# Kernel optimization log

Measured on AMD Instinct MI355X. Metric: run time of the kernel, lower is better.

Reference implementation:

```python
import jax, jax.numpy as jnp
import numpy as np

EPS = 1e-12  # matches torch F.normalize default eps


def _idx(k, pad, stride, size):
    o = (size + 2 * pad - k) // stride + 1
    return (jnp.arange(o) * stride)[:, None] + jnp.arange(k)[None, :], o  # [o, k]


def unfold(x, k, pad, stride):
    # x: [B, C, H, W] -> [B, C*k*k, oh*ow], torch F.unfold ordering (c slowest, then kh, kw)
    B, C, H, W = x.shape
    xp = jnp.pad(x, ((0, 0), (0, 0), (pad, pad), (pad, pad)))
    ri, oh = _idx(k, pad, stride, H)
    ci, ow = _idx(k, pad, stride, W)
    p = xp[:, :, ri[:, None, :, None], ci[None, :, None, :]]  # [B, C, oh, ow, k, k]
    return p.transpose(0, 1, 4, 5, 2, 3).reshape(B, C * k * k, oh * ow)


def fold(cols, out_hw, k, pad, stride):
    # inverse of unfold with overlap-add (torch F.fold)
    B, CKK, L = cols.shape
    C = CKK // (k * k)
    H, W = out_hw
    ri, oh = _idx(k, pad, stride, H)
    ci, ow = _idx(k, pad, stride, W)
    p = cols.reshape(B, C, k, k, oh, ow).transpose(0, 1, 4, 5, 2, 3)  # [B,C,oh,ow,k,k]
    canvas = jnp.zeros((B, C, H + 2 * pad, W + 2 * pad), cols.dtype)
    canvas = canvas.at[:, :, ri[:, None, :, None], ci[None, :, None, :]].add(p)
    return canvas[:, :, pad:pad + H, pad:pad + W]


def _l2norm(x, axis):
    n = jnp.sqrt(jnp.sum(x * x, axis=axis, keepdims=True))
    return x / jnp.maximum(n, EPS)


def setup_inputs() -> dict:
    key = jax.random.key(0)
    ks = jax.random.split(key, 5)
    return {
        "lrsr_lv3": jax.random.normal(ks[0], (1, 256, 48, 48), jnp.float32),
        "refsr_lv3": jax.random.normal(ks[1], (1, 256, 48, 48), jnp.float32),
        "ref_lv1": jax.random.normal(ks[2], (1, 64, 192, 192), jnp.float32),
        "ref_lv2": jax.random.normal(ks[3], (1, 128, 96, 96), jnp.float32),
        "ref_lv3": jax.random.normal(ks[4], (1, 256, 48, 48), jnp.float32),
    }


def reference(lrsr_lv3, refsr_lv3, ref_lv1, ref_lv2, ref_lv3):
    B, C, H, W = lrsr_lv3.shape
    lr_u = unfold(lrsr_lv3, 3, 1, 1)              # [B, C*9, L_lr]
    rf_u = unfold(refsr_lv3, 3, 1, 1)             # [B, C*9, L_ref]
    rf_n = _l2norm(rf_u.transpose(0, 2, 1), 2)    # [B, L_ref, C*9]
    lr_n = _l2norm(lr_u, 1)                       # [B, C*9, L_lr]
    R = jnp.einsum('brc,bcl->brl', rf_n, lr_n)    # [B, L_ref, L_lr] cosine corr
    R_star = jnp.max(R, axis=1)                   # [B, L_lr]
    R_arg = jnp.argmax(R, axis=1)                 # [B, L_lr]

    ref3_u = unfold(ref_lv3, 3, 1, 1)             # [B, C*9,   L_ref]
    ref2_u = unfold(ref_lv2, 6, 2, 2)             # [B, C2*36, L_ref]
    ref1_u = unfold(ref_lv1, 12, 4, 4)            # [B, C1*144,L_ref]

    idx = R_arg[:, None, :]                       # [B, 1, L_lr]
    T3_u = jnp.take_along_axis(ref3_u, idx, axis=2)
    T2_u = jnp.take_along_axis(ref2_u, idx, axis=2)
    T1_u = jnp.take_along_axis(ref1_u, idx, axis=2)

    T_lv3 = fold(T3_u, (H, W), 3, 1, 1) / 9.0
    T_lv2 = fold(T2_u, (H * 2, W * 2), 6, 2, 2) / 9.0
    T_lv1 = fold(T1_u, (H * 4, W * 4), 12, 4, 4) / 9.0
    S = R_star.reshape(B, 1, H, W)
    return (S, T_lv3, T_lv2, T_lv1)
```

## Files before the change

### kernel.cpp

```cpp
#include <hip/hip_runtime.h>
#include <hip/hip_bf16.h>
#include <math.h>

#define HW 48
#define NPOS 2304
#define CCH 256
#define PCOLS 2500
#define PLANESZ (NPOS * CCH)
#define KC 16
#define TM 128
#define TN 64

typedef __attribute__((ext_vector_type(8))) short short8v;
typedef __attribute__((ext_vector_type(16))) float f32x16;

__device__ inline void ph_ss2(int vb, const float* __restrict__ lr,
                              const float* __restrict__ ref, float* __restrict__ SS2,
                              float (*red)[64]) {
    const int img = vb / 36, bx = vb % 36;
    const float* imgp = img ? ref : lr;
    const int t = threadIdx.x;
    const int px = t & 63, cg = t >> 6;
    const int p = bx * 64 + px;
    const float* base = imgp + (size_t)cg * 64 * NPOS + p;
    float s = 0.f;
#pragma unroll 4
    for (int cc = 0; cc < 64; ++cc) {
        float v = base[(size_t)cc * NPOS];
        s = fmaf(v, v, s);
    }
    red[cg][px] = s;
    __syncthreads();
    if (cg == 0)
        SS2[img * NPOS + p] = red[0][px] + red[1][px] + red[2][px] + red[3][px];
}

__device__ inline void ph_split(int local, const float* __restrict__ lr,
                                const float* __restrict__ ref, ushort* __restrict__ planes) {
    const int img = local / 288;
    const int gid = (local % 288) * 256 + threadIdx.x;
    const float* src = img ? ref : lr;
    const int lane = gid & 63;
    const int k16  = (gid >> 6) & 15;
    const int blk  = gid >> 10;
    const int pos  = blk * 32 + (lane & 31);
    const int c0   = k16 * 16 + (lane >> 5) * 8;
    ushort h8[8], m8[8], l8[8];
#pragma unroll
    for (int e = 0; e < 8; ++e) {
        float a = src[(size_t)(c0 + e) * NPOS + pos];
        __hip_bfloat16 hb = __float2bfloat16(a);
        float hf = __bfloat162float(hb);
        float r1 = a - hf;
        __hip_bfloat16 mb = __float2bfloat16(r1);
        float mf = __bfloat162float(mb);
        __hip_bfloat16 lb = __float2bfloat16(r1 - mf);
        h8[e] = *(ushort*)&hb;
        m8[e] = *(ushort*)&mb;
        l8[e] = *(ushort*)&lb;
    }
    ushort* ph = planes + (size_t)(img * 3 + 0) * PLANESZ + (size_t)gid * 8;
    ushort* pm = planes + (size_t)(img * 3 + 1) * PLANESZ + (size_t)gid * 8;
    ushort* pl = planes + (size_t)(img * 3 + 2) * PLANESZ + (size_t)gid * 8;
#pragma unroll
    for (int e = 0; e < 8; ++e) { ph[e] = h8[e]; pm[e] = m8[e]; pl[e] = l8[e]; }
}

__device__ inline void ph_zero(int local, float* __restrict__ P) {
    const int idx = local * 256 + threadIdx.x;
    if (idx >= NPOS * 196) return;
    const int row = idx / 196, b = idx - row * 196;
    int pc;
    if (b < 50)       pc = b;
    else if (b < 100) pc = 2450 + (b - 50);
    else {
        const int i = b - 100;
        const int rr = 1 + (i >> 1);
        pc = rr * 50 + ((i & 1) ? 49 : 0);
    }
    P[(size_t)row * PCOLS + pc] = 0.f;
}

__global__ __launch_bounds__(256) void prep_kernel(const float* __restrict__ lr,
                                                   const float* __restrict__ ref,
                                                   float* __restrict__ SS2,
                                                   ushort* __restrict__ planes,
                                                   float* __restrict__ P,
                                                   int do_split) {
    __shared__ float red[4][64];
    const int b = blockIdx.x;
    if (do_split) {
        if (b < 72)        ph_ss2(b, lr, ref, SS2, red);
        else if (b < 648)  ph_split(b - 72, lr, ref, planes);
        else               ph_zero(b - 648, P);
    } else {
        if (b < 72)        ph_ss2(b, lr, ref, SS2, red);
        else               ph_zero(b - 72, P);
    }
}

__device__ inline void ph_invnorm(int vb, const float* __restrict__ SS2,
                                  float* __restrict__ inv2) {
    const int img = vb / 9;
    const int p = (vb % 9) * 256 + threadIdx.x;
    const float* SS = SS2 + img * NPOS;
    const int y = p / HW, x = p % HW;
    float s = 0.f;
#pragma unroll
    for (int di = -1; di <= 1; ++di) {
        int yy = y + di;
        if ((unsigned)yy >= HW) continue;
#pragma unroll
        for (int dj = -1; dj <= 1; ++dj) {
            int xx = x + dj;
            if ((unsigned)xx >= HW) continue;
            s += SS[yy * HW + xx];
        }
    }
    inv2[img * NPOS + p] = 1.f / fmaxf(sqrtf(s), 1e-12f);
}

__device__ inline void ph_gemm(int g, const ushort* __restrict__ planes,
                               float* __restrict__ P) {
    const int bxg = g % 36, byg = g / 36;
    const int t = threadIdx.x, lane = t & 63, w = t >> 6;
    const int nblk0 = bxg * 2;
    const int ablk  = byg * 4 + w;

    const ushort* baseA  = planes + ((size_t)(ablk * 16) * 64 + lane) * 8;
    const ushort* baseB0 = planes + (size_t)3 * PLANESZ + ((size_t)(nblk0 * 16) * 64 + lane) * 8;
    const ushort* baseB1 = baseB0 + 16 * 64 * 8;

    f32x16 acc0 = {};
    f32x16 acc1 = {};
#pragma unroll 4
    for (int k = 0; k < 16; ++k) {
        const int fo = k * 512;
        short8v ah = *(const short8v*)(baseA + fo);
        short8v am = *(const short8v*)(baseA + PLANESZ + fo);
        short8v al = *(const short8v*)(baseA + 2 * PLANESZ + fo);
        short8v bh0 = *(const short8v*)(baseB0 + fo);
        short8v bm0 = *(const short8v*)(baseB0 + PLANESZ + fo);
        short8v bl0 = *(const short8v*)(baseB0 + 2 * PLANESZ + fo);
        short8v bh1 = *(const short8v*)(baseB1 + fo);
        short8v bm1 = *(const short8v*)(baseB1 + PLANESZ + fo);
        short8v bl1 = *(const short8v*)(baseB1 + 2 * PLANESZ + fo);
        acc0 = __builtin_amdgcn_mfma_f32_32x32x16_bf16(ah, bh0, acc0, 0, 0, 0);
        acc0 = __builtin_amdgcn_mfma_f32_32x32x16_bf16(ah, bm0, acc0, 0, 0, 0);
        acc0 = __builtin_amdgcn_mfma_f32_32x32x16_bf16(am, bh0, acc0, 0, 0, 0);
        acc0 = __builtin_amdgcn_mfma_f32_32x32x16_bf16(ah, bl0, acc0, 0, 0, 0);
        acc0 = __builtin_amdgcn_mfma_f32_32x32x16_bf16(al, bh0, acc0, 0, 0, 0);
        acc0 = __builtin_amdgcn_mfma_f32_32x32x16_bf16(am, bm0, acc0, 0, 0, 0);
        acc1 = __builtin_amdgcn_mfma_f32_32x32x16_bf16(ah, bh1, acc1, 0, 0, 0);
        acc1 = __builtin_amdgcn_mfma_f32_32x32x16_bf16(ah, bm1, acc1, 0, 0, 0);
        acc1 = __builtin_amdgcn_mfma_f32_32x32x16_bf16(am, bh1, acc1, 0, 0, 0);
        acc1 = __builtin_amdgcn_mfma_f32_32x32x16_bf16(ah, bl1, acc1, 0, 0, 0);
        acc1 = __builtin_amdgcn_mfma_f32_32x32x16_bf16(al, bh1, acc1, 0, 0, 0);
        acc1 = __builtin_amdgcn_mfma_f32_32x32x16_bf16(am, bm1, acc1, 0, 0, 0);
    }
    const int m0 = byg * 128 + w * 32;
    const int half = lane >> 5;
    const int colA = nblk0 * 32 + (lane & 31);
    const int colB = colA + 32;
    const int pcA = (colA / 48) * 50 + colA % 48 + 51;
    const int pcB = (colB / 48) * 50 + colB % 48 + 51;
#pragma unroll
    for (int r = 0; r < 16; ++r) {
        const int row = (r & 3) + 8 * (r >> 2) + 4 * half;
        P[(size_t)(m0 + row) * PCOLS + pcA] = acc0[r];
        P[(size_t)(m0 + row) * PCOLS + pcB] = acc1[r];
    }
}

__global__ __launch_bounds__(256) void corr_kernel(const float* __restrict__ SS2,
                                                   float* __restrict__ inv2,
                                                   const ushort* __restrict__ planes,
                                                   float* __restrict__ P,
                                                   int do_gemm) {
    const int b = blockIdx.x;
    if (b < 18)          ph_invnorm(b, SS2, inv2);
    else if (do_gemm)    ph_gemm(b - 18, planes, P);
}

__global__ __launch_bounds__(256) void gemm_p_kernel(const float* __restrict__ lr,
                                                     const float* __restrict__ ref,
                                                     float* __restrict__ P) {
    __shared__ float As[KC][TM];
    __shared__ float Bs[KC][TN];
    const int t  = threadIdx.x;
    const int tx = t & 15, ty = t >> 4;
    const int lp0 = blockIdx.y * TM, rp0 = blockIdx.x * TN;
    const int ac0 = t >> 5,        acol0 = (t & 31) << 2;
    const int ac1 = (t + 256) >> 5, acol1 = acol0;
    const int bc = t >> 4, bcol = (t & 15) << 2;
    float acc[8][4] = {};
    for (int c0 = 0; c0 < CCH; c0 += KC) {
        float4 a0 = *(const float4*)(lr  + (size_t)(c0 + ac0) * NPOS + lp0 + acol0);
        float4 a1 = *(const float4*)(lr  + (size_t)(c0 + ac1) * NPOS + lp0 + acol1);
        float4 b0 = *(const float4*)(ref + (size_t)(c0 + bc)  * NPOS + rp0 + bcol);
        __syncthreads();
        *(float4*)&As[ac0][acol0] = a0;
        *(float4*)&As[ac1][acol1] = a1;
        *(float4*)&Bs[bc][bcol]   = b0;
        __syncthreads();
#pragma unroll
        for (int kk = 0; kk < KC; ++kk) {
            float4 aA = *(const float4*)&As[kk][ty * 8];
            float4 aB = *(const float4*)&As[kk][ty * 8 + 4];
            float4 bb = *(const float4*)&Bs[kk][tx * 4];
            const float av[8] = {aA.x, aA.y, aA.z, aA.w, aB.x, aB.y, aB.z, aB.w};
            const float bv[4] = {bb.x, bb.y, bb.z, bb.w};
#pragma unroll
            for (int i = 0; i < 8; ++i)
#pragma unroll
                for (int j = 0; j < 4; ++j)
                    acc[i][j] = fmaf(av[i], bv[j], acc[i][j]);
        }
    }
    const int col0 = rp0 + tx * 4;
    const int pc0  = (col0 / 48) * 50 + (col0 % 48) + 51;
#pragma unroll
    for (int i = 0; i < 8; ++i) {
        const int m = lp0 + ty * 8 + i;
        float4 v = make_float4(acc[i][0], acc[i][1], acc[i][2], acc[i][3]);
        __builtin_memcpy(P + (size_t)m * PCOLS + pc0, &v, 16);
    }
}

__global__ __launch_bounds__(192) void maxarg_kernel(const float* __restrict__ P,
                                                     const float* __restrict__ inr,
                                                     const float* __restrict__ inl,
                                                     float* __restrict__ S,
                                                     int* __restrict__ arg) {
    const int l  = blockIdx.x;
    const int yl = l / HW, xl = l % HW;
    const int t  = threadIdx.x;

    bool vmask[9];
    const float* bp[9];
#pragma unroll
    for (int d = 0; d < 9; ++d) {
        const int di = d / 3 - 1, dj = d % 3 - 1;
        vmask[d] = ((unsigned)(yl + di) < HW) && ((unsigned)(xl + dj) < HW);
        bp[d] = P + (ptrdiff_t)(l + di * HW + dj) * PCOLS + (di * 50 + dj);
    }

    float best = -1e30f;
    int bestr = 0;
#pragma unroll
    for (int vv = 0; vv < 3; ++vv) {
        const int v   = t + vv * 192;
        const int yr  = v / 12;
        const int xr4 = (v - yr * 12) << 2;
        const int q0  = yr * 50 + xr4 + 51;
        const int r0  = yr * HW + xr4;
        float4 a = make_float4(0.f, 0.f, 0.f, 0.f);
#pragma unroll
        for (int d = 0; d < 9; ++d) {
            if (vmask[d]) {
                float4 x;
                __builtin_memcpy(&x, bp[d] + q0, 16);
                a.x += x.x; a.y += x.y; a.z += x.z; a.w += x.w;
            }
        }
        const float4 w = *(const float4*)(inr + r0);
        const float vals[4] = {a.x * w.x, a.y * w.y, a.z * w.z, a.w * w.w};
#pragma unroll
        for (int k = 0; k < 4; ++k)
            if (vals[k] > best) { best = vals[k]; bestr = r0 + k; }
    }

    __shared__ float bv[256];
    __shared__ int   br[256];
    bv[t] = best; br[t] = bestr;
    if (t < 64) { bv[192 + t] = -1e30f; br[192 + t] = 0; }
    __syncthreads();
    for (int s2 = 128; s2 > 0; s2 >>= 1) {
        if (t < s2) {
            float v2 = bv[t + s2]; int r2 = br[t + s2];
            if (v2 > bv[t] || (v2 == bv[t] && r2 < br[t])) { bv[t] = v2; br[t] = r2; }
        }
        __syncthreads();
    }
    if (t == 0) {
        S[l]   = bv[0] * inl[l];
        arg[l] = br[0];
    }
}

__global__ __launch_bounds__(256) void transposeT_kernel(const float* __restrict__ ref1,
                                                         const float* __restrict__ ref2,
                                                         const float* __restrict__ ref3,
                                                         float* __restrict__ T3t,
                                                         float* __restrict__ T2t,
                                                         float* __restrict__ T1t) {
    __shared__ float tile[64][65];
    const int b = blockIdx.x;
    const float* src; float* dst; int C, NPIX, tpx, tch;
    if (b < 144)      { src = ref3; dst = T3t; C = 256; NPIX = 2304;  tpx = b % 36;  tch = b / 36; }
    else if (b < 432) { const int lb = b - 144; src = ref2; dst = T2t; C = 128; NPIX = 9216;  tpx = lb % 144; tch = lb / 144; }
    else              { const int lb = b - 432; src = ref1; dst = T1t; C = 64;  NPIX = 36864; tpx = lb;       tch = 0; }
    const int t = threadIdx.x;
    const int px0 = tpx * 64, c0 = tch * 64;
#pragma unroll
    for (int r = 0; r < 16; ++r) {
        const int cl = r * 4 + (t >> 6), pl = t & 63;
        tile[cl][pl] = src[(size_t)(c0 + cl) * NPIX + px0 + pl];
    }
    __syncthreads();
#pragma unroll
    for (int r = 0; r < 16; ++r) {
        const int pl = r * 4 + (t >> 6), cl = t & 63;
        dst[(size_t)(px0 + pl) * C + c0 + cl] = tile[cl][pl];
    }
}

template <int S_, int C, int H>
__device__ inline void foldT(const float* __restrict__ refT, const int* __restrict__ arg,
                             float* __restrict__ out, int u, int lane) {
    const int y = u / 48, m = u % 48;
    const int ty_ = y / S_ + 1;
    float4 acc = make_float4(0.f, 0.f, 0.f, 0.f);
#pragma unroll
    for (int a = 0; a < 3; ++a) {
        const int oy = ty_ - a;
        if ((unsigned)oy >= HW) continue;
        const int di = y + S_ - S_ * oy;
#pragma unroll
        for (int b = 0; b < 3; ++b) {
            const int ox = m + 1 - b;
            if ((unsigned)ox >= HW) continue;
            const int ar = arg[oy * HW + ox];
            const int ry = ar / HW, rx = ar % HW;
            const int yy  = S_ * ry + di - S_;
            const int xx0 = S_ * (rx + b - 1);
            if ((unsigned)yy < H && (unsigned)xx0 < H) {
                float4 v;
                __builtin_memcpy(&v, refT + ((size_t)yy * H + xx0) * C + lane * 4, 16);
                acc.x += v.x; acc.y += v.y; acc.z += v.z; acc.w += v.w;
            }
        }
    }
    const int idx = lane * 4;
    const int xx = idx / C;
    const int c  = idx % C;
    const int x  = m * S_ + xx;
    const float vals[4] = {acc.x, acc.y, acc.z, acc.w};
    float* op = out + (size_t)c * (H * H) + (size_t)y * H + x;
#pragma unroll
    for (int e = 0; e < 4; ++e)
        op[(size_t)e * (H * H)] = vals[e] * (1.f / 9.f);
}

__global__ __launch_bounds__(256) void foldT_kernel(const float* __restrict__ T1t,
                                                    const float* __restrict__ T2t,
                                                    const float* __restrict__ T3t,
                                                    const int* __restrict__ argb,
                                                    float* __restrict__ T1,
                                                    float* __restrict__ T2,
                                                    float* __restrict__ T3) {
    const int b = blockIdx.x, w = threadIdx.x >> 6, lane = threadIdx.x & 63;
    if (b < 576)        foldT<1, 256, 48>(T3t, argb, T3, b * 4 + w, lane);
    else if (b < 1728)  foldT<2, 128, 96>(T2t, argb, T2, (b - 576) * 4 + w, lane);
    else                foldT<4, 64, 192>(T1t, argb, T1, (b - 1728) * 4 + w, lane);
}

extern "C" void kernel_launch(void* const* d_in, const int* in_sizes, int n_in,
                              void* d_out, int out_size, void* d_ws, size_t ws_size,
                              hipStream_t stream) {
    const float* lrsr  = (const float*)d_in[0];
    const float* refsr = (const float*)d_in[1];
    const float* ref1  = (const float*)d_in[2];
    const float* ref2  = (const float*)d_in[3];
    const float* ref3  = (const float*)d_in[4];

    float* out = (float*)d_out;
    float* S   = out;
    float* T3  = S  + NPOS;
    float* T2  = T3 + 256 * 48 * 48;
    float* T1  = T2 + 128 * 96 * 96;

    float*  P      = (float*)d_ws;
    float*  SS2    = P + (size_t)NPOS * PCOLS;
    float*  inv2   = SS2 + 2 * NPOS;
    int*    argb   = (int*)(inv2 + 2 * NPOS);
    ushort* planes = (ushort*)(argb + NPOS);
    float*  inl    = inv2;
    float*  inr    = inv2 + NPOS;

    float* T3t = P;
    float* T2t = T3t + 2304 * 256;
    float* T1t = T2t + 9216 * 128;

    const size_t need = ((size_t)NPOS * PCOLS + 5 * NPOS) * 4 + (size_t)6 * PLANESZ * 2;
    const int mfma_path = ws_size >= need ? 1 : 0;

    prep_kernel<<<mfma_path ? 2412 : 1836, 256, 0, stream>>>(lrsr, refsr, SS2, planes, P, mfma_path);

    if (mfma_path) {
        corr_kernel<<<666, 256, 0, stream>>>(SS2, inv2, planes, P, 1);
    } else {
        corr_kernel<<<18, 256, 0, stream>>>(SS2, inv2, planes, P, 0);
        gemm_p_kernel<<<dim3(NPOS / TN, NPOS / TM), 256, 0, stream>>>(lrsr, refsr, P);
    }

    maxarg_kernel<<<NPOS, 192, 0, stream>>>(P, inr, inl, S, argb);

    transposeT_kernel<<<1008, 256, 0, stream>>>(ref1, ref2, ref3, T3t, T2t, T1t);

    foldT_kernel<<<4032, 256, 0, stream>>>(T1t, T2t, T3t, argb, T1, T2, T3);
}
```

Baseline: 88.85 us.

## Fuse reference transpose into prep kernel, shrink GEMM tile, remap maxarg blocks

When the workspace is large enough, the NHWC transposes of ref_lv1/2/3 are placed in their own workspace region and run as extra blocks of the prep kernel, which removes one launch and overlaps them with the prep work. The MFMA GEMM now computes one 32-column block per wave instead of two, doubling the grid to 1296 blocks for better CU occupancy but reloading the A operand twice as often. The maxarg kernel permutes its block-to-position mapping so that consecutive blocks touch different regions of P. Shared memory in prep grows to the size of the transpose tile through a union.

```diff
diff --git a/kernel.cpp b/kernel.cpp
--- a/kernel.cpp
+++ b/kernel.cpp
@@ -81,22 +81,69 @@
     P[(size_t)row * PCOLS + pc] = 0.f;
 }
 
+__device__ inline void ph_transpose(int b, const float* __restrict__ ref1,
+                                    const float* __restrict__ ref2,
+                                    const float* __restrict__ ref3,
+                                    float* __restrict__ T3t, float* __restrict__ T2t,
+                                    float* __restrict__ T1t, float (*tile)[65]) {
+    const float* src; float* dst; int C, NPIX, tpx, tch;
+    if (b < 144)      { src = ref3; dst = T3t; C = 256; NPIX = 2304;  tpx = b % 36;  tch = b / 36; }
+    else if (b < 432) { const int lb = b - 144; src = ref2; dst = T2t; C = 128; NPIX = 9216;  tpx = lb % 144; tch = lb / 144; }
+    else              { const int lb = b - 432; src = ref1; dst = T1t; C = 64;  NPIX = 36864; tpx = lb;       tch = 0; }
+    const int t = threadIdx.x;
+    const int px0 = tpx * 64, c0 = tch * 64;
+#pragma unroll
+    for (int r = 0; r < 16; ++r) {
+        const int cl = r * 4 + (t >> 6), pl = t & 63;
+        tile[cl][pl] = src[(size_t)(c0 + cl) * NPIX + px0 + pl];
+    }
+    __syncthreads();
+#pragma unroll
+    for (int r = 0; r < 16; ++r) {
+        const int pl = r * 4 + (t >> 6), cl = t & 63;
+        dst[(size_t)(px0 + pl) * C + c0 + cl] = tile[cl][pl];
+    }
+}
+
 __global__ __launch_bounds__(256) void prep_kernel(const float* __restrict__ lr,
                                                    const float* __restrict__ ref,
+                                                   const float* __restrict__ ref1,
+                                                   const float* __restrict__ ref2,
+                                                   const float* __restrict__ ref3,
                                                    float* __restrict__ SS2,
                                                    ushort* __restrict__ planes,
                                                    float* __restrict__ P,
-                                                   int do_split) {
-    __shared__ float red[4][64];
+                                                   float* __restrict__ T3t,
+                                                   float* __restrict__ T2t,
+                                                   float* __restrict__ T1t,
+                                                   int do_split, int tbase) {
+    __shared__ union {
+        float red[4][64];
+        float tile[64][65];
+    } sm;
     const int b = blockIdx.x;
+    if (b >= tbase) {
+        ph_transpose(b - tbase, ref1, ref2, ref3, T3t, T2t, T1t, sm.tile);
+        return;
+    }
     if (do_split) {
-        if (b < 72)        ph_ss2(b, lr, ref, SS2, red);
+        if (b < 72)        ph_ss2(b, lr, ref, SS2, sm.red);
         else if (b < 648)  ph_split(b - 72, lr, ref, planes);
         else               ph_zero(b - 648, P);
     } else {
-        if (b < 72)        ph_ss2(b, lr, ref, SS2, red);
+        if (b < 72)        ph_ss2(b, lr, ref, SS2, sm.red);
         else               ph_zero(b - 72, P);
     }
+}
+
+__global__ __launch_bounds__(256) void transposeT_kernel(const float* __restrict__ ref1,
+                                                         const float* __restrict__ ref2,
+                                                         const float* __restrict__ ref3,
+                                                         float* __restrict__ T3t,
+                                                         float* __restrict__ T2t,
+                                                         float* __restrict__ T1t) {
+    __shared__ float tile[64][65];
+    ph_transpose(blockIdx.x, ref1, ref2, ref3, T3t, T2t, T1t, tile);
 }
 
 __device__ inline void ph_invnorm(int vb, const float* __restrict__ SS2,
@@ -122,17 +169,15 @@
 
 __device__ inline void ph_gemm(int g, const ushort* __restrict__ planes,
                                float* __restrict__ P) {
-    const int bxg = g % 36, byg = g / 36;
+    const int bxg = g % 72, byg = g / 72;
     const int t = threadIdx.x, lane = t & 63, w = t >> 6;
-    const int nblk0 = bxg * 2;
+    const int nblk0 = bxg;
     const int ablk  = byg * 4 + w;
 
     const ushort* baseA  = planes + ((size_t)(ablk * 16) * 64 + lane) * 8;
     const ushort* baseB0 = planes + (size_t)3 * PLANESZ + ((size_t)(nblk0 * 16) * 64 + lane) * 8;
-    const ushort* baseB1 = baseB0 + 16 * 64 * 8;
 
     f32x16 acc0 = {};
-    f32x16 acc1 = {};
 #pragma unroll 4
     for (int k = 0; k < 16; ++k) {
         const int fo = k * 512;
@@ -142,33 +187,21 @@
         short8v bh0 = *(const short8v*)(baseB0 + fo);
         short8v bm0 = *(const short8v*)(baseB0 + PLANESZ + fo);
         short8v bl0 = *(const short8v*)(baseB0 + 2 * PLANESZ + fo);
-        short8v bh1 = *(const short8v*)(baseB1 + fo);
-        short8v bm1 = *(const short8v*)(baseB1 + PLANESZ + fo);
-        short8v bl1 = *(const short8v*)(baseB1 + 2 * PLANESZ + fo);
         acc0 = __builtin_amdgcn_mfma_f32_32x32x16_bf16(ah, bh0, acc0, 0, 0, 0);
         acc0 = __builtin_amdgcn_mfma_f32_32x32x16_bf16(ah, bm0, acc0, 0, 0, 0);
         acc0 = __builtin_amdgcn_mfma_f32_32x32x16_bf16(am, bh0, acc0, 0, 0, 0);
         acc0 = __builtin_amdgcn_mfma_f32_32x32x16_bf16(ah, bl0, acc0, 0, 0, 0);
         acc0 = __builtin_amdgcn_mfma_f32_32x32x16_bf16(al, bh0, acc0, 0, 0, 0);
         acc0 = __builtin_amdgcn_mfma_f32_32x32x16_bf16(am, bm0, acc0, 0, 0, 0);
-        acc1 = __builtin_amdgcn_mfma_f32_32x32x16_bf16(ah, bh1, acc1, 0, 0, 0);
-        acc1 = __builtin_amdgcn_mfma_f32_32x32x16_bf16(ah, bm1, acc1, 0, 0, 0);
-        acc1 = __builtin_amdgcn_mfma_f32_32x32x16_bf16(am, bh1, acc1, 0, 0, 0);
-        acc1 = __builtin_amdgcn_mfma_f32_32x32x16_bf16(ah, bl1, acc1, 0, 0, 0);
-        acc1 = __builtin_amdgcn_mfma_f32_32x32x16_bf16(al, bh1, acc1, 0, 0, 0);
-        acc1 = __builtin_amdgcn_mfma_f32_32x32x16_bf16(am, bm1, acc1, 0, 0, 0);
     }
     const int m0 = byg * 128 + w * 32;
     const int half = lane >> 5;
     const int colA = nblk0 * 32 + (lane & 31);
-    const int colB = colA + 32;
     const int pcA = (colA / 48) * 50 + colA % 48 + 51;
-    const int pcB = (colB / 48) * 50 + colB % 48 + 51;
 #pragma unroll
     for (int r = 0; r < 16; ++r) {
         const int row = (r & 3) + 8 * (r >> 2) + 4 * half;
         P[(size_t)(m0 + row) * PCOLS + pcA] = acc0[r];
-        P[(size_t)(m0 + row) * PCOLS + pcB] = acc1[r];
     }
 }
 
@@ -232,7 +265,8 @@
                                                      const float* __restrict__ inl,
                                                      float* __restrict__ S,
                                                      int* __restrict__ arg) {
-    const int l  = blockIdx.x;
+    const int bid = blockIdx.x;
+    const int l   = (bid & 7) * 288 + (bid >> 3);
     const int yl = l / HW, xl = l % HW;
     const int t  = threadIdx.x;
 
@@ -285,33 +319,6 @@
     if (t == 0) {
         S[l]   = bv[0] * inl[l];
         arg[l] = br[0];
-    }
-}
-
-__global__ __launch_bounds__(256) void transposeT_kernel(const float* __restrict__ ref1,
-                                                         const float* __restrict__ ref2,
-                                                         const float* __restrict__ ref3,
-                                                         float* __restrict__ T3t,
-                                                         float* __restrict__ T2t,
-                                                         float* __restrict__ T1t) {
-    __shared__ float tile[64][65];
-    const int b = blockIdx.x;
-    const float* src; float* dst; int C, NPIX, tpx, tch;
-    if (b < 144)      { src = ref3; dst = T3t; C = 256; NPIX = 2304;  tpx = b % 36;  tch = b / 36; }
-    else if (b < 432) { const int lb = b - 144; src = ref2; dst = T2t; C = 128; NPIX = 9216;  tpx = lb % 144; tch = lb / 144; }
-    else              { const int lb = b - 432; src = ref1; dst = T1t; C = 64;  NPIX = 36864; tpx = lb;       tch = 0; }
-    const int t = threadIdx.x;
-    const int px0 = tpx * 64, c0 = tch * 64;
-#pragma unroll
-    for (int r = 0; r < 16; ++r) {
-        const int cl = r * 4 + (t >> 6), pl = t & 63;
-        tile[cl][pl] = src[(size_t)(c0 + cl) * NPIX + px0 + pl];
-    }
-    __syncthreads();
-#pragma unroll
-    for (int r = 0; r < 16; ++r) {
-        const int pl = r * 4 + (t >> 6), cl = t & 63;
-        dst[(size_t)(px0 + pl) * C + c0 + cl] = tile[cl][pl];
     }
 }
 
@@ -388,17 +395,25 @@
     float*  inl    = inv2;
     float*  inr    = inv2 + NPOS;
 
-    float* T3t = P;
+    const size_t need  = ((size_t)NPOS * PCOLS + 5 * NPOS) * 4 + (size_t)6 * PLANESZ * 2;
+    const size_t nhwcB = (size_t)(2304 * 256 + 9216 * 128 + 36864 * 64) * 4;
+    const int mfma_path = ws_size >= need ? 1 : 0;
+    const int bigws     = ws_size >= need + nhwcB ? 1 : 0;
+
+    float* T3t = bigws ? (float*)((char*)d_ws + need) : P;
     float* T2t = T3t + 2304 * 256;
     float* T1t = T2t + 9216 * 128;
 
-    const size_t need = ((size_t)NPOS * PCOLS + 5 * NPOS) * 4 + (size_t)6 * PLANESZ * 2;
-    const int mfma_path = ws_size >= need ? 1 : 0;
-
-    prep_kernel<<<mfma_path ? 2412 : 1836, 256, 0, stream>>>(lrsr, refsr, SS2, planes, P, mfma_path);
+    {
+        const int tbase = mfma_path ? 2412 : 1836;
+        const int grid  = tbase + (bigws ? 1008 : 0);
+        prep_kernel<<<grid, 256, 0, stream>>>(lrsr, refsr, ref1, ref2, ref3,
+                                              SS2, planes, P, T3t, T2t, T1t,
+                                              mfma_path, bigws ? tbase : grid + 1);
+    }
 
     if (mfma_path) {
-        corr_kernel<<<666, 256, 0, stream>>>(SS2, inv2, planes, P, 1);
+        corr_kernel<<<18 + 1296, 256, 0, stream>>>(SS2, inv2, planes, P, 1);
     } else {
         corr_kernel<<<18, 256, 0, stream>>>(SS2, inv2, planes, P, 0);
         gemm_p_kernel<<<dim3(NPOS / TN, NPOS / TM), 256, 0, stream>>>(lrsr, refsr, P);
@@ -406,7 +421,8 @@
 
     maxarg_kernel<<<NPOS, 192, 0, stream>>>(P, inr, inl, S, argb);
 
-    transposeT_kernel<<<1008, 256, 0, stream>>>(ref1, ref2, ref3, T3t, T2t, T1t);
+    if (!bigws)
+        transposeT_kernel<<<1008, 256, 0, stream>>>(ref1, ref2, ref3, T3t, T2t, T1t);
 
     foldT_kernel<<<4032, 256, 0, stream>>>(T1t, T2t, T3t, argb, T1, T2, T3);
 }
```

Measured after the change: 81.54 us (median of 2 runs). 1.09x faster.
